# Performance work log

Measured on AMD Instinct MI355X. Metric: run time of the kernel, lower is better.

The kernel has to match this reference:

```python
import jax, jax.numpy as jnp
import numpy as np

B, N, C, H, KHOP = 8, 1024, 512, 16, 2
HD = C // H
VALID = 768          # valid (non-padded) nodes per batch row
E = B * VALID * 32   # ~deg 32 per valid node
BN_EPS = 1e-5
LN_EPS = 1e-5


def setup_inputs() -> dict:
    key = jax.random.key(0)
    ks = jax.random.split(key, 12)
    x = jax.random.normal(ks[0], (B, N, C), jnp.float32)
    shift = jax.random.normal(ks[1], (B, C), jnp.float32) * 0.1
    scale = jax.random.normal(ks[2], (B, C), jnp.float32) * 0.1
    # fixed-size valid prefix per row -> static shapes under jit
    mask = jnp.broadcast_to(jnp.arange(N) < VALID, (B, N))
    # edges live inside a single graph (same batch row), only among valid nodes,
    # expressed directly in flattened [B*N] index space (== compacted indexing up to relabeling)
    eb = jax.random.randint(ks[3], (E,), 0, B)
    es = jax.random.randint(ks[4], (E,), 0, VALID)
    ed = jax.random.randint(ks[5], (E,), 0, VALID)
    edge_index = jnp.stack([eb * N + es, eb * N + ed]).astype(jnp.int32)
    w = lambda k, s: jax.random.normal(k, s, jnp.float32) * 0.02
    gin_eps = jnp.zeros((KHOP,), jnp.float32)
    gin_w1 = w(ks[6], (KHOP, C, 2 * C)); gin_b1 = jnp.zeros((KHOP, 2 * C), jnp.float32)
    gin_bn_g = jnp.ones((KHOP, 2 * C), jnp.float32); gin_bn_b = jnp.zeros((KHOP, 2 * C), jnp.float32)
    gin_w2 = w(ks[7], (KHOP, 2 * C, C)); gin_b2 = jnp.zeros((KHOP, C), jnp.float32)
    ln_g = jnp.ones((C,), jnp.float32); ln_b = jnp.zeros((C,), jnp.float32)
    qkv_w = w(ks[8], (C, 3 * C)); qkv_b = jnp.zeros((3 * C,), jnp.float32)
    proj_w = w(ks[9], (C, C)); proj_b = jnp.zeros((C,), jnp.float32)
    return dict(x=x, shift=shift, scale=scale, mask=mask, edge_index=edge_index,
                gin_eps=gin_eps, gin_w1=gin_w1, gin_b1=gin_b1, gin_bn_g=gin_bn_g,
                gin_bn_b=gin_bn_b, gin_w2=gin_w2, gin_b2=gin_b2, ln_g=ln_g, ln_b=ln_b,
                qkv_w=qkv_w, qkv_b=qkv_b, proj_w=proj_w, proj_b=proj_b)


def _gin_layer(h, mask_f, cnt, src, dst, eps, w1, b1, g, bt, w2, b2):
    # GINConv: mlp((1+eps)*x_i + sum_{j->i} x_j); MLP = Linear->BatchNorm(batch stats over valid nodes)->ReLU->Linear
    agg = jax.ops.segment_sum(h[src], dst, num_segments=B * N)  # scatter-add messages
    z = (1.0 + eps) * h + agg
    pre = z @ w1 + b1                              # [B*N, 2C]
    mw = mask_f[:, None]
    mean = (pre * mw).sum(0) / cnt                 # masked BN statistics (valid nodes only)
    var = (((pre - mean) ** 2) * mw).sum(0) / cnt  # biased var, as torch BatchNorm
    hn = jax.nn.relu(g * (pre - mean) * jax.lax.rsqrt(var + BN_EPS) + bt)
    return (hn @ w2 + b2) * mw                     # zero out padded nodes (x_struct stays 0 there)


def reference(x, shift, scale, mask, edge_index, gin_eps, gin_w1, gin_b1, gin_bn_g,
              gin_bn_b, gin_w2, gin_b2, ln_g, ln_b, qkv_w, qkv_b, proj_w, proj_b):
    xf = x.reshape(B * N, C)
    mask_f = mask.reshape(-1).astype(x.dtype)
    cnt = mask_f.sum()
    src, dst = edge_index[0], edge_index[1]
    # structure extractor: k-hop GIN with residual after the first hop
    h = _gin_layer(xf * mask_f[:, None], mask_f, cnt, src, dst, gin_eps[0],
                   gin_w1[0], gin_b1[0], gin_bn_g[0], gin_bn_b[0], gin_w2[0], gin_b2[0])
    for i in range(1, KHOP):
        h = _gin_layer(h, mask_f, cnt, src, dst, gin_eps[i],
                       gin_w1[i], gin_b1[i], gin_bn_g[i], gin_bn_b[i], gin_w2[i], gin_b2[i]) + h
    xs = x + h.reshape(B, N, C)  # x + x_struct (x_struct zero on padded nodes)
    # LayerNorm + modulate
    mu = xs.mean(-1, keepdims=True)
    va = xs.var(-1, keepdims=True)
    xn = (xs - mu) * jax.lax.rsqrt(va + LN_EPS) * ln_g + ln_b
    xm = xn * (1.0 + scale[:, None, :]) + shift[:, None, :]
    # SDPA attention with key padding mask
    qkv = (xm @ qkv_w + qkv_b).reshape(B, N, 3, H, HD).transpose(2, 0, 3, 1, 4)
    q, k, v = qkv[0], qkv[1], qkv[2]                       # [B,H,N,HD]
    scores = jnp.einsum('bhqd,bhkd->bhqk', q, k) * (HD ** -0.5)
    scores = scores + jnp.where(mask[:, None, None, :], 0.0, -1e9)
    attn = jax.nn.softmax(scores, axis=-1)
    out = jnp.einsum('bhqk,bhkd->bhqd', attn, v).transpose(0, 2, 1, 3).reshape(B, N, C)
    return out @ proj_w + proj_b
```

## Files before the change

kernel.cpp:

```cpp
#include <hip/hip_runtime.h>
#include <hip/hip_bf16.h>

constexpr int Bc    = 8;
constexpr int Nn    = 1024;
constexpr int Cc    = 512;
constexpr int Hh    = 16;
constexpr int HD    = 32;
constexpr int VALID = 768;
constexpr float CNT_INV = 1.0f / 6144.0f;
constexpr float BN_EPS = 1e-5f;
constexpr float LN_EPS = 1e-5f;
constexpr int ROWS = Bc * Nn;
constexpr int VROWS = Bc * VALID;
constexpr float QSCL = 0.25500526764086547f;

typedef short s16x8 __attribute__((ext_vector_type(8)));
typedef float f32x4 __attribute__((ext_vector_type(4)));

static __device__ __forceinline__ unsigned short f2bf(float f) {
    __hip_bfloat16 h = __float2bfloat16(f);
    return *reinterpret_cast<unsigned short*>(&h);
}
static __device__ __forceinline__ float bf2f(unsigned short u) {
    union { unsigned int u; float f; } c; c.u = (unsigned int)u << 16;
    return c.f;
}
static __device__ __forceinline__ float exp2_fast(float x) {
    float r; asm("v_exp_f32 %0, %1" : "=v"(r) : "v"(x)); return r;
}

static __device__ __forceinline__ int vswz(int d) {
    return ((((d >> 3) ^ (d >> 1)) & 3) << 1) | (d & 1);
}

__global__ __launch_bounds__(256) void k_wt_all(const float* __restrict__ gw1,
                                                const float* __restrict__ gw2,
                                                const float* __restrict__ qkvw,
                                                const float* __restrict__ projw,
                                                const float* __restrict__ x,
                                                unsigned short* __restrict__ w1t,
                                                unsigned short* __restrict__ w2t,
                                                unsigned short* __restrict__ qkvt,
                                                unsigned short* __restrict__ projt,
                                                unsigned short* __restrict__ xb,
                                                float* __restrict__ stats,
                                                int* __restrict__ ideg) {
    const int bi = blockIdx.x;
    if (bi >= 3072) {
        int e = (bi - 3072) * 2048 + threadIdx.x * 8;
        float4 a = *(const float4*)&x[e];
        float4 b = *(const float4*)&x[e + 4];
        s16x8 o;
        o[0] = (short)f2bf(a.x); o[1] = (short)f2bf(a.y);
        o[2] = (short)f2bf(a.z); o[3] = (short)f2bf(a.w);
        o[4] = (short)f2bf(b.x); o[5] = (short)f2bf(b.y);
        o[6] = (short)f2bf(b.z); o[7] = (short)f2bf(b.w);
        *(s16x8*)&xb[e] = o;
        return;
    }
    if (bi == 0) {
        for (int i = threadIdx.x; i < 4096; i += 256) stats[i] = 0.f;
    } else if (bi == 1) {
        for (int i = threadIdx.x; i < 8192; i += 256) ideg[i] = 0;
    }

    const float* W; unsigned short* Wt; int K, N, bx, by;
    if (bi < 1024) {
        int z = bi >> 9, r = bi & 511;
        W = gw1 + (size_t)z * 524288; Wt = w1t + (size_t)z * 524288;
        K = 512; N = 1024; bx = r & 31; by = r >> 5;
    } else if (bi < 2048) {
        int z = (bi - 1024) >> 9, r = (bi - 1024) & 511;
        W = gw2 + (size_t)z * 524288; Wt = w2t + (size_t)z * 524288;
        K = 1024; N = 512; bx = r & 15; by = r >> 4;
    } else if (bi < 2816) {
        int r = bi - 2048;
        W = qkvw; Wt = qkvt; K = 512; N = 1536; bx = r % 48; by = r / 48;
    } else {
        int r = bi - 2816;
        W = projw; Wt = projt; K = 512; N = 512; bx = r & 15; by = r >> 4;
    }

    __shared__ float t[32][33];
    const int k0 = by * 32, n0 = bx * 32;
    int kk = threadIdx.x >> 3, nn = (threadIdx.x & 7) * 4;
    float4 v = *(const float4*)&W[(size_t)(k0 + kk) * N + n0 + nn];
    t[kk][nn] = v.x; t[kk][nn + 1] = v.y; t[kk][nn + 2] = v.z; t[kk][nn + 3] = v.w;
    __syncthreads();
    int nn2 = threadIdx.x >> 3, kk2 = (threadIdx.x & 7) * 4;
    ushort4 o;
    o.x = f2bf(t[kk2][nn2]);     o.y = f2bf(t[kk2 + 1][nn2]);
    o.z = f2bf(t[kk2 + 2][nn2]); o.w = f2bf(t[kk2 + 3][nn2]);
    *(ushort4*)&Wt[(size_t)(n0 + nn2) * K + k0 + kk2] = o;
}

__global__ __launch_bounds__(256) void k_count(const int* __restrict__ ei,
                                               int* __restrict__ deg, int E) {
    int e = blockIdx.x * 256 + threadIdx.x;
    if (e < E) atomicAdd(&deg[ei[E + e]], 1);
}

__global__ __launch_bounds__(1024) void k_scan(const int* __restrict__ deg,
                                               int* __restrict__ start,
                                               int* __restrict__ cursor) {
    __shared__ int csum[1024];
    const int t = threadIdx.x;
    const int base = t * 8;
    int local[8];
    int s = 0;
#pragma unroll
    for (int i = 0; i < 8; ++i) { local[i] = deg[base + i]; s += local[i]; }
    csum[t] = s;
    __syncthreads();
    for (int off = 1; off < 1024; off <<= 1) {
        int v = (t >= off) ? csum[t - off] : 0;
        __syncthreads();
        if (t >= off) csum[t] += v;
        __syncthreads();
    }
    int excl = (t == 0) ? 0 : csum[t - 1];
#pragma unroll
    for (int i = 0; i < 8; ++i) {
        start[base + i]  = excl;
        cursor[base + i] = excl;
        excl += local[i];
    }
    if (t == 1023) start[8192] = excl;
}

__global__ __launch_bounds__(256) void k_fill(const int* __restrict__ ei,
                                              int* __restrict__ cursor,
                                              int* __restrict__ list, int E) {
    int e = blockIdx.x * 256 + threadIdx.x;
    if (e < E) {
        int pos = atomicAdd(&cursor[ei[E + e]], 1);
        list[pos] = ei[e];
    }
}

__global__ __launch_bounds__(64) void k_gather_z(const unsigned short* __restrict__ h,
                                                 const int* __restrict__ start,
                                                 const int* __restrict__ list,
                                                 const float* __restrict__ epsArr,
                                                 int layer,
                                                 unsigned short* __restrict__ z) {
    const int vr = blockIdx.x;
    const int batch = vr / 768;
    const int row = batch * 1024 + (vr - batch * 768);
    const int c = threadIdx.x * 8;
    const int s0 = start[row], s1 = start[row + 1];
    const float e1 = 1.0f + epsArr[layer];
    const unsigned short* hp = h + c;
    s16x8 bv = *(const s16x8*)&h[(size_t)row * 512 + c];
    float a[8];
#pragma unroll
    for (int i = 0; i < 8; ++i) a[i] = bf2f((unsigned short)bv[i]) * e1;
    int j = s0;
    for (; j + 4 <= s1; j += 4) {
        int sA = list[j], sB = list[j + 1], sC = list[j + 2], sD = list[j + 3];
        s16x8 vA = *(const s16x8*)&hp[(size_t)sA * 512];
        s16x8 vB = *(const s16x8*)&hp[(size_t)sB * 512];
        s16x8 vC = *(const s16x8*)&hp[(size_t)sC * 512];
        s16x8 vD = *(const s16x8*)&hp[(size_t)sD * 512];
#pragma unroll
        for (int i = 0; i < 8; ++i) {
            a[i] += bf2f((unsigned short)vA[i]);
            a[i] += bf2f((unsigned short)vB[i]);
            a[i] += bf2f((unsigned short)vC[i]);
            a[i] += bf2f((unsigned short)vD[i]);
        }
    }
    for (; j < s1; ++j) {
        s16x8 vA = *(const s16x8*)&hp[(size_t)list[j] * 512];
#pragma unroll
        for (int i = 0; i < 8; ++i) a[i] += bf2f((unsigned short)vA[i]);
    }
    s16x8 o;
#pragma unroll
    for (int i = 0; i < 8; ++i) o[i] = (short)f2bf(a[i]);
    *(s16x8*)&z[(size_t)row * 512 + c] = o;
}

template <bool RESIDUAL, bool STATS, bool SKIPM, bool OUTBF, bool QSCALE,
          bool HBF, bool SKIPKV>
__global__ __launch_bounds__(256) void k_gemm_bf(const unsigned short* __restrict__ A,
                                                 const unsigned short* __restrict__ Bt,
                                                 const float* __restrict__ bias,
                                                 const float* __restrict__ res,
                                                 void* __restrict__ Cd,
                                                 float* __restrict__ stats,
                                                 unsigned short* __restrict__ hb,
                                                 int K, int Nc) {
    __shared__ unsigned short Al[128 * 64];
    __shared__ unsigned short Bl[128 * 64];
    const int tid  = threadIdx.x;
    const int by   = blockIdx.y;
    const int bm   = SKIPM ? ((by / 6) * 1024 + (by % 6) * 128) : (by * 128);
    const int bn   = blockIdx.x * 128;
    if (SKIPKV && (by & 7) >= 6 && bn >= 512) return;
    const int wid  = tid >> 6, lane = tid & 63;
    const int wr   = wid >> 1, wc = wid & 1;
    const int lo16 = lane & 15, g = lane >> 4;

    const int sr = tid >> 1;
    const int sh = tid & 1;
    const size_t a_off = (size_t)(bm + sr) * K + sh * 32;
    const size_t b_off = (size_t)(bn + sr) * K + sh * 32;

    f32x4 acc[4][4];
#pragma unroll
    for (int m = 0; m < 4; ++m)
#pragma unroll
        for (int n = 0; n < 4; ++n) acc[m][n] = (f32x4){0.f, 0.f, 0.f, 0.f};

    const int NT = K >> 6;
    s16x8 ar[4], br[4];
    {
        const s16x8* ap = (const s16x8*)(A + a_off);
        const s16x8* bp = (const s16x8*)(Bt + b_off);
#pragma unroll
        for (int i = 0; i < 4; ++i) { ar[i] = ap[i]; br[i] = bp[i]; }
    }

    for (int kt = 0; kt < NT; ++kt) {
        __syncthreads();
#pragma unroll
        for (int i = 0; i < 4; ++i) {
            int sl = (sh * 4 + i) ^ (sr & 7);
            *(s16x8*)&Al[sr * 64 + sl * 8] = ar[i];
            *(s16x8*)&Bl[sr * 64 + sl * 8] = br[i];
        }
        __syncthreads();
        if (kt + 1 < NT) {
            const s16x8* ap = (const s16x8*)(A + a_off + (size_t)(kt + 1) * 64);
            const s16x8* bp = (const s16x8*)(Bt + b_off + (size_t)(kt + 1) * 64);
#pragma unroll
            for (int i = 0; i < 4; ++i) { ar[i] = ap[i]; br[i] = bp[i]; }
        }
#pragma unroll
        for (int ks = 0; ks < 2; ++ks) {
            s16x8 af[4], bfr[4];
#pragma unroll
            for (int m = 0; m < 4; ++m) {
                int r = wr * 64 + m * 16 + lo16;
                int sl = (ks * 4 + g) ^ (r & 7);
                af[m] = *(const s16x8*)&Al[r * 64 + sl * 8];
            }
#pragma unroll
            for (int n = 0; n < 4; ++n) {
                int r = wc * 64 + n * 16 + lo16;
                int sl = (ks * 4 + g) ^ (r & 7);
                bfr[n] = *(const s16x8*)&Bl[r * 64 + sl * 8];
            }
            __builtin_amdgcn_s_setprio(1);
#pragma unroll
            for (int m = 0; m < 4; ++m)
#pragma unroll
                for (int n = 0; n < 4; ++n)
                    acc[m][n] = __builtin_amdgcn_mfma_f32_16x16x32_bf16(
                        af[m], bfr[n], acc[m][n], 0, 0, 0);
            __builtin_amdgcn_s_setprio(0);
        }
    }

#pragma unroll
    for (int n = 0; n < 4; ++n) {
        int col = bn + wc * 64 + n * 16 + lo16;
        float bb = bias[col];
        bool qs = QSCALE && (col < 512);
        float s = 0.f, s2 = 0.f;
#pragma unroll
        for (int m = 0; m < 4; ++m) {
#pragma unroll
            for (int ri = 0; ri < 4; ++ri) {
                int row = bm + wr * 64 + m * 16 + g * 4 + ri;
                float v = acc[m][n][ri] + bb;
                if (STATS) { s += v; s2 += v * v; }
                if (RESIDUAL) v += res[(size_t)row * Nc + col];
                if (QSCALE && qs) v *= QSCL;
                if (OUTBF) ((unsigned short*)Cd)[(size_t)row * Nc + col] = f2bf(v);
                else       ((float*)Cd)[(size_t)row * Nc + col] = v;
                if (HBF)   hb[(size_t)row * Nc + col] = f2bf(v);
            }
        }
        if (STATS) {
            s  += __shfl_xor(s, 16);  s  += __shfl_xor(s, 32);
            s2 += __shfl_xor(s2, 16); s2 += __shfl_xor(s2, 32);
            if (g == 0) {
                atomicAdd(&stats[col], s);
                atomicAdd(&stats[1024 + col], s2);
            }
        }
    }
}

__global__ __launch_bounds__(128) void k_bn_apply(const unsigned short* __restrict__ pre,
                                                  const float* __restrict__ stats,
                                                  const float* __restrict__ g,
                                                  const float* __restrict__ bt,
                                                  unsigned short* __restrict__ hn) {
    const int vr = blockIdx.x;
    const int batch = vr / 768;
    const int row = batch * 1024 + (vr - batch * 768);
    const int c0 = threadIdx.x * 8;
    const size_t off = (size_t)row * 1024 + c0;
    s16x8 v = *(const s16x8*)&pre[off];
    s16x8 o;
#pragma unroll
    for (int i = 0; i < 8; ++i) {
        float sm = stats[c0 + i], sq = stats[1024 + c0 + i];
        float m = sm * CNT_INV;
        float r = rsqrtf(sq * CNT_INV - m * m + BN_EPS);
        float hv = g[c0 + i] * (bf2f((unsigned short)v[i]) - m) * r + bt[c0 + i];
        o[i] = (short)f2bf(fmaxf(hv, 0.f));
    }
    *(s16x8*)&hn[off] = o;
}

__global__ __launch_bounds__(256) void k_ln_mod(const float* __restrict__ x,
                                                const float* __restrict__ h,
                                                const float* __restrict__ lg,
                                                const float* __restrict__ lb,
                                                const float* __restrict__ sc,
                                                const float* __restrict__ sh,
                                                unsigned short* __restrict__ xm) {
    int row  = blockIdx.x * 4 + (threadIdx.x >> 6);
    int lane = threadIdx.x & 63;
    const size_t base = (size_t)row * 512 + lane * 8;
    const bool val = (row & 1023) < VALID;

    float v[8];
    float4 a0 = *(const float4*)&x[base],     a1 = *(const float4*)&x[base + 4];
    float4 b0 = *(const float4*)&h[base],     b1 = *(const float4*)&h[base + 4];
    if (!val) { b0.x=b0.y=b0.z=b0.w=0.f; b1.x=b1.y=b1.z=b1.w=0.f; }
    v[0] = a0.x + b0.x; v[1] = a0.y + b0.y; v[2] = a0.z + b0.z; v[3] = a0.w + b0.w;
    v[4] = a1.x + b1.x; v[5] = a1.y + b1.y; v[6] = a1.z + b1.z; v[7] = a1.w + b1.w;

    float s = 0.f, s2 = 0.f;
#pragma unroll
    for (int j = 0; j < 8; ++j) { s += v[j]; s2 += v[j] * v[j]; }
#pragma unroll
    for (int off = 32; off; off >>= 1) {
        s  += __shfl_xor(s, off);
        s2 += __shfl_xor(s2, off);
    }
    float mu  = s * (1.0f / 512.0f);
    float var = s2 * (1.0f / 512.0f) - mu * mu;
    float rs  = rsqrtf(var + LN_EPS);

    int c0 = lane * 8;
    int bidx = row >> 10;
    const float* scp = sc + (size_t)bidx * 512 + c0;
    const float* shp = sh + (size_t)bidx * 512 + c0;
    s16x8 o;
#pragma unroll
    for (int j = 0; j < 8; ++j) {
        float xn = (v[j] - mu) * rs * lg[c0 + j] + lb[c0 + j];
        o[j] = (short)f2bf(xn * (1.0f + scp[j]) + shp[j]);
    }
    *(s16x8*)&xm[base] = o;
}

__global__ __launch_bounds__(256) void k_attn_mfma(const unsigned short* __restrict__ qkv,
                                                   unsigned short* __restrict__ att) {
    __shared__ __align__(16) unsigned short Kl[128 * 32];
    __shared__ __align__(16) unsigned short Vt[32 * 128];
    __shared__ __align__(16) unsigned short Pl[4][16 * 128];

    const int w    = threadIdx.x >> 6;
    const int lane = threadIdx.x & 63;
    const int bh   = blockIdx.x;
    const int b    = bh >> 4, h = bh & 15;
    const int qt   = blockIdx.y;
    const int lo16 = lane & 15;
    const int g    = lane >> 4;

    s16x8 qf[2];
#pragma unroll
    for (int qi = 0; qi < 2; ++qi) {
        int qrow = qt * 128 + qi * 64 + w * 16 + lo16;
        qf[qi] = *(const s16x8*)&qkv[(size_t)(b * 1024 + qrow) * 1536 + h * 32 + g * 8];
    }

    f32x4 o0[2] = {{0.f,0.f,0.f,0.f},{0.f,0.f,0.f,0.f}};
    f32x4 o1[2] = {{0.f,0.f,0.f,0.f},{0.f,0.f,0.f,0.f}};
    float l_run[2] = {0.f, 0.f};

    const size_t kvbase = (size_t)(b * 1024) * 1536 + h * 32;

    const int kr_r = threadIdx.x >> 2;
    const int kr_g = threadIdx.x & 3;
    const int vk0  = (threadIdx.x >> 2) * 2;
    const int vgg  = threadIdx.x & 3;

    s16x8 kA, kB, vA, vB;
    {
        const unsigned short* kp = &qkv[kvbase + (size_t)kr_r * 1536 + 512 + kr_g * 8];
        kA = *(const s16x8*)kp;
        kB = *(const s16x8*)(kp + (size_t)64 * 1536);
        const unsigned short* vp = &qkv[kvbase + (size_t)vk0 * 1536 + 1024 + vgg * 8];
        vA = *(const s16x8*)vp;
        vB = *(const s16x8*)(vp + 1536);
    }

    for (int kc = 0; kc < VALID; kc += 128) {
        __syncthreads();

        {
            int slot = kr_g ^ ((kr_r >> 1) & 3);
            *(s16x8*)&Kl[kr_r * 32 + slot * 8] = kA;
            int r2 = 64 + kr_r;
            slot = kr_g ^ ((r2 >> 1) & 3);
            *(s16x8*)&Kl[r2 * 32 + slot * 8] = kB;
        }
#pragma unroll
        for (int j = 0; j < 8; ++j) {
            int d = vgg * 8 + j;
            int slot = (vk0 >> 3) ^ vswz(d);
            int elem = d * 128 + slot * 8 + (vk0 & 7);
            unsigned int pack = (unsigned int)(unsigned short)vA[j] |
                                ((unsigned int)(unsigned short)vB[j] << 16);
            *(unsigned int*)&Vt[elem] = pack;
        }
        __syncthreads();

        if (kc + 128 < VALID) {
            const unsigned short* kp = &qkv[kvbase + (size_t)(kc + 128 + kr_r) * 1536 + 512 + kr_g * 8];
            kA = *(const s16x8*)kp;
            kB = *(const s16x8*)(kp + (size_t)64 * 1536);
            const unsigned short* vp = &qkv[kvbase + (size_t)(kc + 128 + vk0) * 1536 + 1024 + vgg * 8];
            vA = *(const s16x8*)vp;
            vB = *(const s16x8*)(vp + 1536);
        }

#pragma unroll
        for (int qi = 0; qi < 2; ++qi) {
            f32x4 sc[8];
            __builtin_amdgcn_s_setprio(1);
#pragma unroll
            for (int t = 0; t < 8; ++t) {
                int r = t * 16 + lo16;
                int slot = g ^ ((r >> 1) & 3);
                s16x8 kf = *(const s16x8*)&Kl[r * 32 + slot * 8];
                f32x4 z = {0.f, 0.f, 0.f, 0.f};
                sc[t] = __builtin_amdgcn_mfma_f32_16x16x32_bf16(kf, qf[qi], z, 0, 0, 0);
            }
            __builtin_amdgcn_s_setprio(0);

            float lsum = 0.f;
#pragma unroll
            for (int t = 0; t < 8; ++t) {
                float p0 = exp2_fast(sc[t][0]);
                float p1 = exp2_fast(sc[t][1]);
                float p2 = exp2_fast(sc[t][2]);
                float p3 = exp2_fast(sc[t][3]);
                lsum += (p0 + p1) + (p2 + p3);
                int kstart = t * 16 + g * 4;
                int slot = (kstart >> 3) ^ (lo16 & 7);
                int elem = lo16 * 128 + slot * 8 + (kstart & 7);
                unsigned int lo = (unsigned int)f2bf(p0) | ((unsigned int)f2bf(p1) << 16);
                unsigned int hi = (unsigned int)f2bf(p2) | ((unsigned int)f2bf(p3) << 16);
                uint2 pk; pk.x = lo; pk.y = hi;
                *(uint2*)&Pl[w][elem] = pk;
            }
            l_run[qi] += lsum;

            asm volatile("s_waitcnt lgkmcnt(0)" ::: "memory");
            __builtin_amdgcn_sched_barrier(0);

            __builtin_amdgcn_s_setprio(1);
#pragma unroll
            for (int sub = 0; sub < 4; ++sub) {
                int slotp = (sub * 4 + g) ^ (lo16 & 7);
                s16x8 pa = *(const s16x8*)&Pl[w][lo16 * 128 + slotp * 8];
                int d0 = lo16;
                s16x8 vb0 = *(const s16x8*)&Vt[d0 * 128 + (((sub * 4 + g) ^ vswz(d0)) * 8)];
                int d1 = 16 + lo16;
                s16x8 vb1 = *(const s16x8*)&Vt[d1 * 128 + (((sub * 4 + g) ^ vswz(d1)) * 8)];
                o0[qi] = __builtin_amdgcn_mfma_f32_16x16x32_bf16(pa, vb0, o0[qi], 0, 0, 0);
                o1[qi] = __builtin_amdgcn_mfma_f32_16x16x32_bf16(pa, vb1, o1[qi], 0, 0, 0);
            }
            __builtin_amdgcn_s_setprio(0);
        }
    }

#pragma unroll
    for (int qi = 0; qi < 2; ++qi) {
        float l = l_run[qi];
        l += __shfl_xor(l, 16);
        l += __shfl_xor(l, 32);
#pragma unroll
        for (int r = 0; r < 4; ++r) {
            float lr = __shfl(l, g * 4 + r);
            float inv = 1.f / lr;
            int qq = qt * 128 + qi * 64 + w * 16 + g * 4 + r;
            unsigned short* op = att + ((size_t)(b * 1024 + qq) * 512 + h * 32);
            op[lo16]      = f2bf(o0[qi][r] * inv);
            op[16 + lo16] = f2bf(o1[qi][r] * inv);
        }
    }
}

extern "C" void kernel_launch(void* const* d_in, const int* in_sizes, int n_in,
                              void* d_out, int out_size, void* d_ws, size_t ws_size,
                              hipStream_t stream) {
    const float* x     = (const float*)d_in[0];
    const float* shift = (const float*)d_in[1];
    const float* scale = (const float*)d_in[2];
    const int*   ei    = (const int*)d_in[4];
    const float* geps  = (const float*)d_in[5];
    const float* gw1   = (const float*)d_in[6];
    const float* gb1   = (const float*)d_in[7];
    const float* gbg   = (const float*)d_in[8];
    const float* gbb   = (const float*)d_in[9];
    const float* gw2   = (const float*)d_in[10];
    const float* gb2   = (const float*)d_in[11];
    const float* lng   = (const float*)d_in[12];
    const float* lnb   = (const float*)d_in[13];
    const float* qkvw  = (const float*)d_in[14];
    const float* qkvb  = (const float*)d_in[15];
    const float* projw = (const float*)d_in[16];
    const float* projb = (const float*)d_in[17];
    const int E = in_sizes[4] / 2;

    float* ws    = (float*)d_ws;
    float* bufA  = ws;
    float* bufB  = ws + 4194304;
    float* preq  = ws + 8388608;
    float* stats = ws + 20971520;
    int*   ideg    = (int*)(ws + 20975616);
    int*   istart  = ideg + 8192;
    int*   icursor = istart + 8193;
    int*   ilist   = icursor + 8192;
    unsigned short* hnb = (unsigned short*)(ws + 16777216);
    unsigned short* wts = (unsigned short*)(ws + 21200896);
    unsigned short* w1t   = wts;
    unsigned short* w2t   = wts + 1048576;
    unsigned short* qkvt  = wts + 2097152;
    unsigned short* projt = wts + 2883584;
    unsigned short* xb  = (unsigned short*)preq;
    unsigned short* hb  = (unsigned short*)(preq + 2097152);
    unsigned short* pre = (unsigned short*)preq;

    k_wt_all<<<5120, 256, 0, stream>>>(gw1, gw2, qkvw, projw, x,
                                       w1t, w2t, qkvt, projt, xb, stats, ideg);

    k_count<<<(E + 255) / 256, 256, 0, stream>>>(ei, ideg, E);
    k_scan<<<1, 1024, 0, stream>>>(ideg, istart, icursor);
    k_fill<<<(E + 255) / 256, 256, 0, stream>>>(ei, icursor, ilist, E);

    for (int layer = 0; layer < 2; ++layer) {
        const unsigned short* hin = layer ? hb : xb;
        unsigned short* zb = (unsigned short*)(layer ? bufA : bufB);
        float* st = stats + layer * 2048;
        k_gather_z<<<VROWS, 64, 0, stream>>>(hin, istart, ilist, geps, layer, zb);
        k_gemm_bf<false, true, true, true, false, false, false>
            <<<dim3(8, 48), 256, 0, stream>>>(
            zb, w1t + (size_t)layer * 524288, gb1 + layer * 1024, nullptr,
            pre, st, nullptr, 512, 1024);
        k_bn_apply<<<VROWS, 128, 0, stream>>>(pre, st, gbg + layer * 1024,
                                              gbb + layer * 1024, hnb);
        if (layer == 0) {
            k_gemm_bf<false, false, true, false, false, true, false>
                <<<dim3(4, 48), 256, 0, stream>>>(
                hnb, w2t, gb2, nullptr, bufB, nullptr, hb, 1024, 512);
        } else {
            k_gemm_bf<true, false, true, false, false, false, false>
                <<<dim3(4, 48), 256, 0, stream>>>(
                hnb, w2t + 524288, gb2 + 512, bufB, bufA, nullptr, nullptr, 1024, 512);
        }
    }

    unsigned short* xmb = (unsigned short*)bufB;
    k_ln_mod<<<2048, 256, 0, stream>>>(x, bufA, lng, lnb, scale, shift, xmb);
    unsigned short* qkvb16 = (unsigned short*)preq;
    k_gemm_bf<false, false, false, true, true, false, true>
        <<<dim3(12, 64), 256, 0, stream>>>(
        xmb, qkvt, qkvb, nullptr, qkvb16, nullptr, nullptr, 512, 1536);
    unsigned short* attb = (unsigned short*)bufA;
    k_attn_mfma<<<dim3(128, 8), 256, 0, stream>>>(qkvb16, attb);
    k_gemm_bf<false, false, false, false, false, false, false>
        <<<dim3(4, 64), 256, 0, stream>>>(
        attb, projt, projb, nullptr, (float*)d_out, nullptr, nullptr, 512, 512);
}
```

Baseline: 231.8 us.

## Add narrow-N GEMM tiles for small GEMMs and interleave attention query halves

The bf16 GEMM takes a template tile width. The GIN MLP GEMMs and the output projection now use 128x64 tiles, which doubles the grid so more blocks fill the CUs; the QKV GEMM keeps 128x128. The attention kernel is unrolled by hand so that the second query half's score MFMAs are issued before the first half's P·V, with the loop array state turned into named scalars. The aim is to hide exp and LDS latency behind MFMA work. The cost is less reuse per tile in the narrow GEMMs and higher register pressure in attention.

```diff
diff --git a/kernel.cpp b/kernel.cpp
--- a/kernel.cpp
+++ b/kernel.cpp
@@ -182,7 +182,7 @@
 }
 
 template <bool RESIDUAL, bool STATS, bool SKIPM, bool OUTBF, bool QSCALE,
-          bool HBF, bool SKIPKV>
+          bool HBF, bool SKIPKV, int BNSZ>
 __global__ __launch_bounds__(256) void k_gemm_bf(const unsigned short* __restrict__ A,
                                                  const unsigned short* __restrict__ Bt,
                                                  const float* __restrict__ bias,
@@ -192,34 +192,39 @@
                                                  unsigned short* __restrict__ hb,
                                                  int K, int Nc) {
     __shared__ unsigned short Al[128 * 64];
-    __shared__ unsigned short Bl[128 * 64];
+    __shared__ unsigned short Bl[BNSZ * 64];
+    constexpr int NF = BNSZ / 32;
+    constexpr int NB = (BNSZ == 128) ? 4 : 2;
     const int tid  = threadIdx.x;
     const int by   = blockIdx.y;
     const int bm   = SKIPM ? ((by / 6) * 1024 + (by % 6) * 128) : (by * 128);
-    const int bn   = blockIdx.x * 128;
+    const int bn   = blockIdx.x * BNSZ;
     if (SKIPKV && (by & 7) >= 6 && bn >= 512) return;
     const int wid  = tid >> 6, lane = tid & 63;
     const int wr   = wid >> 1, wc = wid & 1;
     const int lo16 = lane & 15, g = lane >> 4;
 
-    const int sr = tid >> 1;
-    const int sh = tid & 1;
+    const int sr = tid >> 1, sh = tid & 1;
     const size_t a_off = (size_t)(bm + sr) * K + sh * 32;
-    const size_t b_off = (size_t)(bn + sr) * K + sh * 32;
-
-    f32x4 acc[4][4];
+    const int srb = (BNSZ == 128) ? (tid >> 1) : (tid >> 2);
+    const int shb = (BNSZ == 128) ? (tid & 1)  : (tid & 3);
+    const size_t b_off = (size_t)(bn + srb) * K + shb * (BNSZ == 128 ? 32 : 16);
+
+    f32x4 acc[4][NF];
 #pragma unroll
     for (int m = 0; m < 4; ++m)
 #pragma unroll
-        for (int n = 0; n < 4; ++n) acc[m][n] = (f32x4){0.f, 0.f, 0.f, 0.f};
+        for (int n = 0; n < NF; ++n) acc[m][n] = (f32x4){0.f, 0.f, 0.f, 0.f};
 
     const int NT = K >> 6;
-    s16x8 ar[4], br[4];
+    s16x8 ar[4], br[NB];
     {
         const s16x8* ap = (const s16x8*)(A + a_off);
         const s16x8* bp = (const s16x8*)(Bt + b_off);
 #pragma unroll
-        for (int i = 0; i < 4; ++i) { ar[i] = ap[i]; br[i] = bp[i]; }
+        for (int i = 0; i < 4; ++i)  ar[i] = ap[i];
+#pragma unroll
+        for (int i = 0; i < NB; ++i) br[i] = bp[i];
     }
 
     for (int kt = 0; kt < NT; ++kt) {
@@ -228,18 +233,25 @@
         for (int i = 0; i < 4; ++i) {
             int sl = (sh * 4 + i) ^ (sr & 7);
             *(s16x8*)&Al[sr * 64 + sl * 8] = ar[i];
-            *(s16x8*)&Bl[sr * 64 + sl * 8] = br[i];
+        }
+#pragma unroll
+        for (int i = 0; i < NB; ++i) {
+            int s = (BNSZ == 128) ? (shb * 4 + i) : (shb * 2 + i);
+            int sl = s ^ (srb & 7);
+            *(s16x8*)&Bl[srb * 64 + sl * 8] = br[i];
         }
         __syncthreads();
         if (kt + 1 < NT) {
             const s16x8* ap = (const s16x8*)(A + a_off + (size_t)(kt + 1) * 64);
             const s16x8* bp = (const s16x8*)(Bt + b_off + (size_t)(kt + 1) * 64);
 #pragma unroll
-            for (int i = 0; i < 4; ++i) { ar[i] = ap[i]; br[i] = bp[i]; }
+            for (int i = 0; i < 4; ++i)  ar[i] = ap[i];
+#pragma unroll
+            for (int i = 0; i < NB; ++i) br[i] = bp[i];
         }
 #pragma unroll
         for (int ks = 0; ks < 2; ++ks) {
-            s16x8 af[4], bfr[4];
+            s16x8 af[4], bfr[NF];
 #pragma unroll
             for (int m = 0; m < 4; ++m) {
                 int r = wr * 64 + m * 16 + lo16;
@@ -247,8 +259,8 @@
                 af[m] = *(const s16x8*)&Al[r * 64 + sl * 8];
             }
 #pragma unroll
-            for (int n = 0; n < 4; ++n) {
-                int r = wc * 64 + n * 16 + lo16;
+            for (int n = 0; n < NF; ++n) {
+                int r = wc * (BNSZ / 2) + n * 16 + lo16;
                 int sl = (ks * 4 + g) ^ (r & 7);
                 bfr[n] = *(const s16x8*)&Bl[r * 64 + sl * 8];
             }
@@ -256,7 +268,7 @@
 #pragma unroll
             for (int m = 0; m < 4; ++m)
 #pragma unroll
-                for (int n = 0; n < 4; ++n)
+                for (int n = 0; n < NF; ++n)
                     acc[m][n] = __builtin_amdgcn_mfma_f32_16x16x32_bf16(
                         af[m], bfr[n], acc[m][n], 0, 0, 0);
             __builtin_amdgcn_s_setprio(0);
@@ -264,8 +276,8 @@
     }
 
 #pragma unroll
-    for (int n = 0; n < 4; ++n) {
-        int col = bn + wc * 64 + n * 16 + lo16;
+    for (int n = 0; n < NF; ++n) {
+        int col = bn + wc * (BNSZ / 2) + n * 16 + lo16;
         float bb = bias[col];
         bool qs = QSCALE && (col < 512);
         float s = 0.f, s2 = 0.f;
@@ -375,16 +387,13 @@
     const int lo16 = lane & 15;
     const int g    = lane >> 4;
 
-    s16x8 qf[2];
-#pragma unroll
-    for (int qi = 0; qi < 2; ++qi) {
-        int qrow = qt * 128 + qi * 64 + w * 16 + lo16;
-        qf[qi] = *(const s16x8*)&qkv[(size_t)(b * 1024 + qrow) * 1536 + h * 32 + g * 8];
-    }
-
-    f32x4 o0[2] = {{0.f,0.f,0.f,0.f},{0.f,0.f,0.f,0.f}};
-    f32x4 o1[2] = {{0.f,0.f,0.f,0.f},{0.f,0.f,0.f,0.f}};
-    float l_run[2] = {0.f, 0.f};
+    const int qrowA = qt * 128 + w * 16 + lo16;
+    s16x8 qfa = *(const s16x8*)&qkv[(size_t)(b * 1024 + qrowA) * 1536 + h * 32 + g * 8];
+    s16x8 qfb = *(const s16x8*)&qkv[(size_t)(b * 1024 + qrowA + 64) * 1536 + h * 32 + g * 8];
+
+    f32x4 o0a = {0.f,0.f,0.f,0.f}, o1a = {0.f,0.f,0.f,0.f};
+    f32x4 o0b = {0.f,0.f,0.f,0.f}, o1b = {0.f,0.f,0.f,0.f};
+    float la = 0.f, lb = 0.f;
 
     const size_t kvbase = (size_t)(b * 1024) * 1536 + h * 32;
 
@@ -433,20 +442,19 @@
             vB = *(const s16x8*)(vp + 1536);
         }
 
-#pragma unroll
-        for (int qi = 0; qi < 2; ++qi) {
-            f32x4 sc[8];
-            __builtin_amdgcn_s_setprio(1);
-#pragma unroll
-            for (int t = 0; t < 8; ++t) {
-                int r = t * 16 + lo16;
-                int slot = g ^ ((r >> 1) & 3);
-                s16x8 kf = *(const s16x8*)&Kl[r * 32 + slot * 8];
-                f32x4 z = {0.f, 0.f, 0.f, 0.f};
-                sc[t] = __builtin_amdgcn_mfma_f32_16x16x32_bf16(kf, qf[qi], z, 0, 0, 0);
-            }
-            __builtin_amdgcn_s_setprio(0);
-
+        f32x4 sc[8];
+        __builtin_amdgcn_s_setprio(1);
+#pragma unroll
+        for (int t = 0; t < 8; ++t) {
+            int r = t * 16 + lo16;
+            int slot = g ^ ((r >> 1) & 3);
+            s16x8 kf = *(const s16x8*)&Kl[r * 32 + slot * 8];
+            f32x4 z = {0.f, 0.f, 0.f, 0.f};
+            sc[t] = __builtin_amdgcn_mfma_f32_16x16x32_bf16(kf, qfa, z, 0, 0, 0);
+        }
+        __builtin_amdgcn_s_setprio(0);
+
+        {
             float lsum = 0.f;
 #pragma unroll
             for (int t = 0; t < 8; ++t) {
@@ -463,30 +471,79 @@
                 uint2 pk; pk.x = lo; pk.y = hi;
                 *(uint2*)&Pl[w][elem] = pk;
             }
-            l_run[qi] += lsum;
-
-            asm volatile("s_waitcnt lgkmcnt(0)" ::: "memory");
-            __builtin_amdgcn_sched_barrier(0);
-
-            __builtin_amdgcn_s_setprio(1);
-#pragma unroll
-            for (int sub = 0; sub < 4; ++sub) {
-                int slotp = (sub * 4 + g) ^ (lo16 & 7);
-                s16x8 pa = *(const s16x8*)&Pl[w][lo16 * 128 + slotp * 8];
-                int d0 = lo16;
-                s16x8 vb0 = *(const s16x8*)&Vt[d0 * 128 + (((sub * 4 + g) ^ vswz(d0)) * 8)];
-                int d1 = 16 + lo16;
-                s16x8 vb1 = *(const s16x8*)&Vt[d1 * 128 + (((sub * 4 + g) ^ vswz(d1)) * 8)];
-                o0[qi] = __builtin_amdgcn_mfma_f32_16x16x32_bf16(pa, vb0, o0[qi], 0, 0, 0);
-                o1[qi] = __builtin_amdgcn_mfma_f32_16x16x32_bf16(pa, vb1, o1[qi], 0, 0, 0);
+            la += lsum;
+        }
+
+        f32x4 sd[8];
+        __builtin_amdgcn_s_setprio(1);
+#pragma unroll
+        for (int t = 0; t < 8; ++t) {
+            int r = t * 16 + lo16;
+            int slot = g ^ ((r >> 1) & 3);
+            s16x8 kf = *(const s16x8*)&Kl[r * 32 + slot * 8];
+            f32x4 z = {0.f, 0.f, 0.f, 0.f};
+            sd[t] = __builtin_amdgcn_mfma_f32_16x16x32_bf16(kf, qfb, z, 0, 0, 0);
+        }
+        __builtin_amdgcn_s_setprio(0);
+
+        asm volatile("s_waitcnt lgkmcnt(0)" ::: "memory");
+        __builtin_amdgcn_sched_barrier(0);
+
+        __builtin_amdgcn_s_setprio(1);
+#pragma unroll
+        for (int sub = 0; sub < 4; ++sub) {
+            int slotp = (sub * 4 + g) ^ (lo16 & 7);
+            s16x8 pa = *(const s16x8*)&Pl[w][lo16 * 128 + slotp * 8];
+            int d0 = lo16;
+            s16x8 vb0 = *(const s16x8*)&Vt[d0 * 128 + (((sub * 4 + g) ^ vswz(d0)) * 8)];
+            int d1 = 16 + lo16;
+            s16x8 vb1 = *(const s16x8*)&Vt[d1 * 128 + (((sub * 4 + g) ^ vswz(d1)) * 8)];
+            o0a = __builtin_amdgcn_mfma_f32_16x16x32_bf16(pa, vb0, o0a, 0, 0, 0);
+            o1a = __builtin_amdgcn_mfma_f32_16x16x32_bf16(pa, vb1, o1a, 0, 0, 0);
+        }
+        __builtin_amdgcn_s_setprio(0);
+
+        {
+            float lsum = 0.f;
+#pragma unroll
+            for (int t = 0; t < 8; ++t) {
+                float p0 = exp2_fast(sd[t][0]);
+                float p1 = exp2_fast(sd[t][1]);
+                float p2 = exp2_fast(sd[t][2]);
+                float p3 = exp2_fast(sd[t][3]);
+                lsum += (p0 + p1) + (p2 + p3);
+                int kstart = t * 16 + g * 4;
+                int slot = (kstart >> 3) ^ (lo16 & 7);
+                int elem = lo16 * 128 + slot * 8 + (kstart & 7);
+                unsigned int lo = (unsigned int)f2bf(p0) | ((unsigned int)f2bf(p1) << 16);
+                unsigned int hi = (unsigned int)f2bf(p2) | ((unsigned int)f2bf(p3) << 16);
+                uint2 pk; pk.x = lo; pk.y = hi;
+                *(uint2*)&Pl[w][elem] = pk;
             }
-            __builtin_amdgcn_s_setprio(0);
-        }
+            lb += lsum;
+        }
+
+        asm volatile("s_waitcnt lgkmcnt(0)" ::: "memory");
+        __builtin_amdgcn_sched_barrier(0);
+
+        __builtin_amdgcn_s_setprio(1);
+#pragma unroll
+        for (int sub = 0; sub < 4; ++sub) {
+            int slotp = (sub * 4 + g) ^ (lo16 & 7);
+            s16x8 pa = *(const s16x8*)&Pl[w][lo16 * 128 + slotp * 8];
+            int d0 = lo16;
+            s16x8 vb0 = *(const s16x8*)&Vt[d0 * 128 + (((sub * 4 + g) ^ vswz(d0)) * 8)];
+            int d1 = 16 + lo16;
+            s16x8 vb1 = *(const s16x8*)&Vt[d1 * 128 + (((sub * 4 + g) ^ vswz(d1)) * 8)];
+            o0b = __builtin_amdgcn_mfma_f32_16x16x32_bf16(pa, vb0, o0b, 0, 0, 0);
+            o1b = __builtin_amdgcn_mfma_f32_16x16x32_bf16(pa, vb1, o1b, 0, 0, 0);
+        }
+        __builtin_amdgcn_s_setprio(0);
     }
 
 #pragma unroll
     for (int qi = 0; qi < 2; ++qi) {
-        float l = l_run[qi];
+        float l = qi ? lb : la;
         l += __shfl_xor(l, 16);
         l += __shfl_xor(l, 32);
 #pragma unroll
@@ -495,8 +552,10 @@
             float inv = 1.f / lr;
             int qq = qt * 128 + qi * 64 + w * 16 + g * 4 + r;
             unsigned short* op = att + ((size_t)(b * 1024 + qq) * 512 + h * 32);
-            op[lo16]      = f2bf(o0[qi][r] * inv);
-            op[16 + lo16] = f2bf(o1[qi][r] * inv);
+            float v0 = (qi ? o0b[r] : o0a[r]) * inv;
+            float v1 = (qi ? o1b[r] : o1a[r]) * inv;
+            op[lo16]      = f2bf(v0);
+            op[16 + lo16] = f2bf(v1);
         }
     }
 }
@@ -554,19 +613,19 @@
         unsigned short* zb = (unsigned short*)(layer ? bufA : bufB);
         float* st = stats + layer * 2048;
         k_gather_z<<<VROWS, 64, 0, stream>>>(hin, istart, ilist, geps, layer, zb);
-        k_gemm_bf<false, true, true, true, false, false, false>
-            <<<dim3(8, 48), 256, 0, stream>>>(
+        k_gemm_bf<false, true, true, true, false, false, false, 64>
+            <<<dim3(16, 48), 256, 0, stream>>>(
             zb, w1t + (size_t)layer * 524288, gb1 + layer * 1024, nullptr,
             pre, st, nullptr, 512, 1024);
         k_bn_apply<<<VROWS, 128, 0, stream>>>(pre, st, gbg + layer * 1024,
                                               gbb + layer * 1024, hnb);
         if (layer == 0) {
-            k_gemm_bf<false, false, true, false, false, true, false>
-                <<<dim3(4, 48), 256, 0, stream>>>(
+            k_gemm_bf<false, false, true, false, false, true, false, 64>
+                <<<dim3(8, 48), 256, 0, stream>>>(
                 hnb, w2t, gb2, nullptr, bufB, nullptr, hb, 1024, 512);
         } else {
-            k_gemm_bf<true, false, true, false, false, false, false>
-                <<<dim3(4, 48), 256, 0, stream>>>(
+            k_gemm_bf<true, false, true, false, false, false, false, 64>
+                <<<dim3(8, 48), 256, 0, stream>>>(
                 hnb, w2t + 524288, gb2 + 512, bufB, bufA, nullptr, nullptr, 1024, 512);
         }
     }
@@ -574,12 +633,12 @@
     unsigned short* xmb = (unsigned short*)bufB;
     k_ln_mod<<<2048, 256, 0, stream>>>(x, bufA, lng, lnb, scale, shift, xmb);
     unsigned short* qkvb16 = (unsigned short*)preq;
-    k_gemm_bf<false, false, false, true, true, false, true>
+    k_gemm_bf<false, false, false, true, true, false, true, 128>
         <<<dim3(12, 64), 256, 0, stream>>>(
         xmb, qkvt, qkvb, nullptr, qkvb16, nullptr, nullptr, 512, 1536);
     unsigned short* attb = (unsigned short*)bufA;
     k_attn_mfma<<<dim3(128, 8), 256, 0, stream>>>(qkvb16, attb);
-    k_gemm_bf<false, false, false, false, false, false, false>
-        <<<dim3(4, 64), 256, 0, stream>>>(
+    k_gemm_bf<false, false, false, false, false, false, false, 64>
+        <<<dim3(8, 64), 256, 0, stream>>>(
         attb, projt, projb, nullptr, (float*)d_out, nullptr, nullptr, 512, 512);
 }
```

Result: no change. 230.1 us (-0.7%).
